# Performance work log

Measured on AMD Instinct MI355X. Metric: run time of the kernel, lower is better.

Reference implementation:

```python
import jax, jax.numpy as jnp
import numpy as np

B, T, C = 4, 2048, 1024


def wkv(k, v, w, u, reverse):
    """RWKV WKV scan with running-max stabilization.
    k, v: [B, T, C]; w, u: [C]. Returns y: [B, T, C]."""
    def step(carry, kv):
        num, den, mx = carry          # each [B, C]
        k_t, v_t = kv                 # each [B, C]
        ku = k_t + u
        m = jnp.maximum(mx, ku)
        e1 = jnp.exp(mx - m)
        e2 = jnp.exp(ku - m)
        y = (e1 * num + e2 * v_t) / (e1 * den + e2)
        # state update with decay w
        mw = mx + w
        mn = jnp.maximum(mw, k_t)
        e1s = jnp.exp(mw - mn)
        e2s = jnp.exp(k_t - mn)
        return (e1s * num + e2s * v_t, e1s * den + e2s, mn), y

    z = jnp.zeros_like(k[:, 0])
    init = (z, z, jnp.full_like(z, -1e38))
    ks = jnp.swapaxes(k, 0, 1)  # [T, B, C]
    vs = jnp.swapaxes(v, 0, 1)
    _, ys = jax.lax.scan(step, init, (ks, vs), reverse=reverse)
    return jnp.swapaxes(ys, 0, 1)


def setup_inputs() -> dict:
    key = jax.random.key(0)
    k1, k2, k3, k4, k5, k6, k7 = jax.random.split(key, 7)
    x = jax.random.normal(k1, (B, T, C), dtype=jnp.float32)
    rkv_w = jax.random.normal(k2, (6 * C, C), dtype=jnp.float32) / np.sqrt(C)
    out_w = jax.random.normal(k3, (C, 2 * C), dtype=jnp.float32) / np.sqrt(2 * C)
    time_decay = jax.random.uniform(k4, (C,), jnp.float32, -6.0, -5.0)
    time_first = jax.random.uniform(k5, (C,), jnp.float32, -3.0, 0.0)
    time_decay_rev = jax.random.uniform(k6, (C,), jnp.float32, -6.0, -5.0)
    time_first_rev = jax.random.uniform(k7, (C,), jnp.float32, -3.0, 0.0)
    return {"x": x, "rkv_w": rkv_w, "out_w": out_w,
            "time_decay": time_decay, "time_first": time_first,
            "time_decay_rev": time_decay_rev, "time_first_rev": time_first_rev}


def reference(x, rkv_w, out_w, time_decay, time_first, time_decay_rev, time_first_rev):
    b, t, c = x.shape
    rkv = jnp.einsum('btc,dc->btd', x, rkv_w).reshape(b, t, 2, 3, c)
    r_f, k_f, v_f = rkv[:, :, 0, 0], rkv[:, :, 0, 1], rkv[:, :, 0, 2]
    r_b, k_b, v_b = rkv[:, :, 1, 0], rkv[:, :, 1, 1], rkv[:, :, 1, 2]
    out_f = jax.nn.sigmoid(r_f) * wkv(k_f, v_f, -jnp.exp(time_decay), time_first, False)
    out_b = jax.nn.sigmoid(r_b) * wkv(k_b, v_b, -jnp.exp(time_decay_rev), time_first_rev, True)
    out_cat = jnp.concatenate([out_f, out_b], axis=-1)  # [B, T, 2C]
    return jnp.einsum('btd,cd->btc', out_cat, out_w)
```

## Files before the change

### kernel.cpp

```cpp
#include <hip/hip_runtime.h>
#include <cstdint>
#include <cstddef>

#define Bdim 4
#define Tdim 2048
#define Cdim 1024

#define SEG  32
#define CHB  32
#define LSEG (Tdim / SEG)

#define G1_K    1024
#define G1_GX   24
#define G1_CPX  96
#define G1_NIPT 8
#define G1_NITER 24
#define G1_GMAX 47

typedef __attribute__((ext_vector_type(8))) short bf16x8;
typedef __attribute__((ext_vector_type(4))) float f32x4;

__device__ __forceinline__ unsigned short f2bf(float f) {
    unsigned int u = __float_as_uint(f);
    u += 0x7fffu + ((u >> 16) & 1u);
    return (unsigned short)(u >> 16);
}
__device__ __forceinline__ float bf2f(unsigned short h) {
    return __uint_as_float((unsigned int)h << 16);
}

__device__ __forceinline__ void gload_lds16(const void* g, void* l) {
    __builtin_amdgcn_global_load_lds(
        (const __attribute__((address_space(1))) unsigned int*)g,
        (__attribute__((address_space(3))) unsigned int*)l,
        16, 0, 0);
}

__global__ __launch_bounds__(256) void cast_f32_bf16(
    const float* __restrict__ in, unsigned short* __restrict__ out, int n4)
{
    int i = blockIdx.x * 256 + threadIdx.x;
    if (i >= n4) return;
    float4 v = ((const float4*)in)[i];
    ushort4 o;
    o.x = f2bf(v.x); o.y = f2bf(v.y); o.z = f2bf(v.z); o.w = f2bf(v.w);
    ((ushort4*)out)[i] = o;
}

__device__ __forceinline__ void stage_half(
    const unsigned short* __restrict__ G, int row0, int K, int elemoff,
    char* slot, int wave, int lane)
{
    const int sl = (lane & 3) ^ ((lane >> 3) & 3);
    const unsigned short* gp = G + (size_t)(row0 + wave * 16 + (lane >> 2)) * K
                                 + elemoff + sl * 8;
    gload_lds16(gp, slot + wave * 1024);
    gload_lds16(gp + (size_t)128 * K, slot + 8192 + wave * 1024);
}

#define GP(D, KH, MH, GPTR, ROW0, ELEMOFF, SSLOT, VM)                          \
  {                                                                            \
    const char* As_ = ldsb + (D)*32768 + (KH)*16384;                           \
    const char* Bs_ = ldsb + 65536 + (D)*32768 + (KH)*16384;                   \
    bf16x8 a_[4], b_[4];                                                       \
    _Pragma("unroll")                                                          \
    for (int i_ = 0; i_ < 4; ++i_)                                             \
      a_[i_] = *(const bf16x8*)(As_ + (wm*128 + ((MH)*4+i_)*16 + fr)*64 + cswz);\
    _Pragma("unroll")                                                          \
    for (int j_ = 0; j_ < 4; ++j_)                                             \
      b_[j_] = *(const bf16x8*)(Bs_ + (wn*64 + j_*16 + fr)*64 + cswz);         \
    stage_half(GPTR, ROW0, G1_K, ELEMOFF, SSLOT, wave, lane);                  \
    __builtin_amdgcn_s_barrier();                                              \
    __builtin_amdgcn_sched_barrier(0);                                         \
    __builtin_amdgcn_s_setprio(1);                                             \
    _Pragma("unroll")                                                          \
    for (int i_ = 0; i_ < 4; ++i_)                                             \
      _Pragma("unroll")                                                        \
      for (int j_ = 0; j_ < 4; ++j_)                                           \
        acc[(MH)*4+i_][j_] = __builtin_amdgcn_mfma_f32_16x16x32_bf16(          \
            a_[i_], b_[j_], acc[(MH)*4+i_][j_], 0, 0, 0);                      \
    __builtin_amdgcn_s_setprio(0);                                             \
    if (VM) { asm volatile("s_waitcnt vmcnt(8)" ::: "memory"); }               \
    __builtin_amdgcn_s_barrier();                                              \
    __builtin_amdgcn_sched_barrier(0);                                         \
  }

#define SELJ(j, a0, a1, a2) ((j) == 0 ? (a0) : ((j) == 1 ? (a1) : (a2)))

__global__ __launch_bounds__(512, 1) void gemm1_persist(
    const unsigned short* __restrict__ A, const unsigned short* __restrict__ B,
    unsigned short* __restrict__ C, int N)
{
    __shared__ char ldsbuf[131072];
    char* ldsb = ldsbuf;

    const int tid  = threadIdx.x;
    const int wave = tid >> 6;
    const int lane = tid & 63;
    const int wm = wave >> 2;
    const int wn = wave & 3;
    const int fr = lane & 15;
    const int cswz = (((lane >> 4) ^ ((fr >> 1) & 3)) << 4);

    int m0j[1], n0j[1];
    int m0_0, n0_0, m0_1, n0_1, m0_2, n0_2;
    {
        int vb, swz;
        vb = blockIdx.x;          swz = (vb & 7) * G1_CPX + (vb >> 3);
        m0_0 = (swz / G1_GX) * 256; n0_0 = (swz % G1_GX) * 256;
        vb = blockIdx.x + 256;    swz = (vb & 7) * G1_CPX + (vb >> 3);
        m0_1 = (swz / G1_GX) * 256; n0_1 = (swz % G1_GX) * 256;
        vb = blockIdx.x + 512;    swz = (vb & 7) * G1_CPX + (vb >> 3);
        m0_2 = (swz / G1_GX) * 256; n0_2 = (swz % G1_GX) * 256;
    }
    (void)m0j; (void)n0j;

    f32x4 acc[8][4] = {};

    stage_half(A, m0_0, G1_K, 0,  ldsb + 0,             wave, lane);
    stage_half(B, n0_0, G1_K, 0,  ldsb + 65536,         wave, lane);
    stage_half(A, m0_0, G1_K, 32, ldsb + 16384,         wave, lane);
    stage_half(B, n0_0, G1_K, 32, ldsb + 65536 + 16384, wave, lane);
    stage_half(A, m0_0, G1_K, 64, ldsb + 32768,         wave, lane);
    stage_half(B, n0_0, G1_K, 64, ldsb + 65536 + 32768, wave, lane);
    asm volatile("s_waitcnt vmcnt(8)" ::: "memory");
    __builtin_amdgcn_s_barrier();
    __builtin_amdgcn_sched_barrier(0);

    for (int i = 0; i < G1_NITER; ++i) {
        const int jc  = i >> 3;
        int g2 = 2 * i + 2; if (g2 > G1_GMAX) g2 = G1_GMAX;
        int g3 = 2 * i + 3; if (g3 > G1_GMAX) g3 = G1_GMAX;
        const int j2 = g2 >> 4, kt2 = g2 & 15;
        const int j3 = g3 >> 4, kt3 = g3 & 15;
        const int kt1 = (2 * i + 1) & 15;

        const int m0c = SELJ(jc, m0_0, m0_1, m0_2);
        const int n0c = SELJ(jc, n0_0, n0_1, n0_2);
        const int m02 = SELJ(j2, m0_0, m0_1, m0_2);
        const int n02 = SELJ(j2, n0_0, n0_1, n0_2);
        const int m03 = SELJ(j3, m0_0, m0_1, m0_2);
        const int n03 = SELJ(j3, n0_0, n0_1, n0_2);

        GP(0, 0, 0, A, m0c, kt1 * 64 + 32, ldsb + 32768 + 16384,         0)
        GP(0, 0, 1, B, n0c, kt1 * 64 + 32, ldsb + 65536 + 32768 + 16384, 1)
        GP(0, 1, 0, A, m02, kt2 * 64,      ldsb + 0,                     0)
        GP(0, 1, 1, B, n02, kt2 * 64,      ldsb + 65536,                 1)
        GP(1, 0, 0, A, m02, kt2 * 64 + 32, ldsb + 16384,                 0)
        GP(1, 0, 1, B, n02, kt2 * 64 + 32, ldsb + 65536 + 16384,         1)
        GP(1, 1, 0, A, m03, kt3 * 64,      ldsb + 32768,                 0)
        GP(1, 1, 1, B, n03, kt3 * 64,      ldsb + 65536 + 32768,         1)

        if ((i & 7) == 7) {
            #pragma unroll
            for (int mi = 0; mi < 8; ++mi) {
                const int row = m0c + wm * 128 + mi * 16 + (lane >> 4) * 4;
                #pragma unroll
                for (int nj = 0; nj < 4; ++nj) {
                    const int col = n0c + wn * 64 + nj * 16 + fr;
                    #pragma unroll
                    for (int r = 0; r < 4; ++r)
                        C[(size_t)(row + r) * N + col] = f2bf(acc[mi][nj][r]);
                }
            }
            #pragma unroll
            for (int mi = 0; mi < 8; ++mi)
                #pragma unroll
                for (int nj = 0; nj < 4; ++nj)
                    acc[mi][nj] = (f32x4){0.f, 0.f, 0.f, 0.f};
        }
    }
}

__global__ __launch_bounds__(256) void gemm_bf16_nt(
    const unsigned short* __restrict__ A, const unsigned short* __restrict__ B,
    float* __restrict__ C, int M, int N, int K)
{
    __shared__ unsigned short As[128 * 32];
    __shared__ unsigned short Bs[128 * 32];

    const int tid  = threadIdx.x;
    const int wave = tid >> 6;
    const int lane = tid & 63;
    const int m0 = blockIdx.y * 128;
    const int n0 = blockIdx.x * 128;
    const int wr = wave >> 1, wc = wave & 1;

    const int srow = tid >> 2;
    const int scol = (tid & 3) * 8;
    const unsigned short* Ag = A + (size_t)(m0 + srow) * K + scol;
    const unsigned short* Bg = B + (size_t)(n0 + srow) * K + scol;
    char* AsW = (char*)As + wave * 1024;
    char* BsW = (char*)Bs + wave * 1024;

    f32x4 acc[4][4] = {};

    const int fr = lane & 15;
    const int fk = (lane >> 4) * 8;

    for (int k0 = 0; k0 < K; k0 += 32) {
        gload_lds16(Ag + k0,                  AsW);
        gload_lds16(Ag + k0 + (size_t)64 * K, AsW + 4096);
        gload_lds16(Bg + k0,                  BsW);
        gload_lds16(Bg + k0 + (size_t)64 * K, BsW + 4096);
        __syncthreads();

        bf16x8 af[4], bfr_[4];
        #pragma unroll
        for (int f = 0; f < 4; ++f) {
            af[f]   = *(const bf16x8*)&As[(wr * 64 + f * 16 + fr) * 32 + fk];
            bfr_[f] = *(const bf16x8*)&Bs[(wc * 64 + f * 16 + fr) * 32 + fk];
        }
        #pragma unroll
        for (int i = 0; i < 4; ++i)
            #pragma unroll
            for (int j = 0; j < 4; ++j)
                acc[i][j] = __builtin_amdgcn_mfma_f32_16x16x32_bf16(
                    af[i], bfr_[j], acc[i][j], 0, 0, 0);
        __syncthreads();
    }

    #pragma unroll
    for (int i = 0; i < 4; ++i) {
        const int row = m0 + wr * 64 + i * 16 + (lane >> 4) * 4;
        #pragma unroll
        for (int j = 0; j < 4; ++j) {
            const int col = n0 + wc * 64 + j * 16 + (lane & 15);
            #pragma unroll
            for (int r = 0; r < 4; ++r)
                C[(size_t)(row + r) * N + col] = acc[i][j][r];
        }
    }
}

__global__ __launch_bounds__(1024) void wkv_scan_par(
    const unsigned short* __restrict__ rkv,
    const float* __restrict__ td,  const float* __restrict__ tf,
    const float* __restrict__ tdr, const float* __restrict__ tfr,
    unsigned short* __restrict__ outcat)
{
    __shared__ float sBn[SEG][CHB], sBd[SEG][CHB], sMb[SEG][CHB];

    const int tid = threadIdx.x;
    const int ch  = tid & (CHB - 1);
    const int seg = tid >> 5;

    const int bi  = blockIdx.x;
    const int b   = bi >> 6;
    const int rem = bi & 63;
    const int dir = rem >> 5;
    const int c   = (rem & 31) * CHB + ch;

    const float w = -__expf(dir ? tdr[c] : td[c]);
    const float u = dir ? tfr[c] : tf[c];

    const int strideT = 6 * Cdim;
    const int tstep   = dir ? -strideT : strideT;
    const int t0      = dir ? (Tdim - 1 - seg * LSEG) : (seg * LSEG);

    const unsigned short* pbase = rkv + ((size_t)b * Tdim + t0) * strideT + dir * 3 * Cdim + c;

    const int PF = 8;

    float bn = 0.0f, bd = 0.0f, mb = -1e38f;
    {
        const unsigned short* q = pbase;
        float kk[PF], vv[PF];
        #pragma unroll
        for (int i = 0; i < PF; ++i) {
            kk[i] = bf2f(q[Cdim]); vv[i] = bf2f(q[2 * Cdim]); q += tstep;
        }
        for (int t = 0; t < LSEG; t += PF) {
            float kn[PF], vn[PF];
            if (t + PF < LSEG) {
                #pragma unroll
                for (int i = 0; i < PF; ++i) {
                    kn[i] = bf2f(q[Cdim]); vn[i] = bf2f(q[2 * Cdim]); q += tstep;
                }
            }
            #pragma unroll
            for (int i = 0; i < PF; ++i) {
                const float k_ = kk[i], v_ = vv[i];
                const float mw = mb + w;
                const float mn = fmaxf(mw, k_);
                const float e1 = __expf(mw - mn);
                const float e2 = __expf(k_ - mn);
                bn = e1 * bn + e2 * v_;
                bd = e1 * bd + e2;
                mb = mn;
            }
            #pragma unroll
            for (int i = 0; i < PF; ++i) { kk[i] = kn[i]; vv[i] = vn[i]; }
        }
    }
    sBn[seg][ch] = bn; sBd[seg][ch] = bd; sMb[seg][ch] = mb;
    __syncthreads();

    if (tid < CHB) {
        float n = 0.0f, d = 0.0f, m = -1e38f;
        const float a = w * (float)LSEG;
        for (int s = 0; s < SEG; ++s) {
            const float tn = sBn[s][tid], tdn = sBd[s][tid], tm = sMb[s][tid];
            sBn[s][tid] = n; sBd[s][tid] = d; sMb[s][tid] = m;
            const float ma = m + a;
            const float mm = fmaxf(ma, tm);
            const float e1 = __expf(ma - mm);
            const float e2 = __expf(tm - mm);
            n = e1 * n + e2 * tn;
            d = e1 * d + e2 * tdn;
            m = mm;
        }
    }
    __syncthreads();

    float num = sBn[seg][ch], den = sBd[seg][ch], mx = sMb[seg][ch];
    {
        const unsigned short* q = pbase;
        unsigned short* po = outcat + ((size_t)b * Tdim + t0) * (2 * Cdim) + dir * Cdim + c;
        const int ostep = dir ? -(2 * Cdim) : (2 * Cdim);

        float rr[PF], kk[PF], vv[PF];
        #pragma unroll
        for (int i = 0; i < PF; ++i) {
            rr[i] = bf2f(q[0]); kk[i] = bf2f(q[Cdim]); vv[i] = bf2f(q[2 * Cdim]); q += tstep;
        }
        for (int t = 0; t < LSEG; t += PF) {
            float rn[PF], kn[PF], vn[PF];
            if (t + PF < LSEG) {
                #pragma unroll
                for (int i = 0; i < PF; ++i) {
                    rn[i] = bf2f(q[0]); kn[i] = bf2f(q[Cdim]); vn[i] = bf2f(q[2 * Cdim]); q += tstep;
                }
            }
            #pragma unroll
            for (int i = 0; i < PF; ++i) {
                const float k_ = kk[i], v_ = vv[i], r_ = rr[i];
                const float ku = k_ + u;
                const float m  = fmaxf(mx, ku);
                const float e1 = __expf(mx - m);
                const float e2 = __expf(ku - m);
                const float y  = (e1 * num + e2 * v_) / (e1 * den + e2);
                const float sr = 1.0f / (1.0f + __expf(-r_));
                *po = f2bf(sr * y);
                po += ostep;
                const float mw  = mx + w;
                const float mn  = fmaxf(mw, k_);
                const float e1s = __expf(mw - mn);
                const float e2s = __expf(k_ - mn);
                num = e1s * num + e2s * v_;
                den = e1s * den + e2s;
                mx  = mn;
            }
            #pragma unroll
            for (int i = 0; i < PF; ++i) { rr[i] = rn[i]; kk[i] = kn[i]; vv[i] = vn[i]; }
        }
    }
}

extern "C" void kernel_launch(void* const* d_in, const int* in_sizes, int n_in,
                              void* d_out, int out_size, void* d_ws, size_t ws_size,
                              hipStream_t stream)
{
    const float* x    = (const float*)d_in[0];
    const float* rkvw = (const float*)d_in[1];
    const float* outw = (const float*)d_in[2];
    const float* td   = (const float*)d_in[3];
    const float* tf   = (const float*)d_in[4];
    const float* tdr  = (const float*)d_in[5];
    const float* tfr  = (const float*)d_in[6];
    float* out = (float*)d_out;

    const int M = Bdim * Tdim;

    char* ws = (char*)d_ws;
    unsigned short* rkv = (unsigned short*)ws;
    unsigned short* xb  = (unsigned short*)(ws + 100663296);
    unsigned short* wb  = (unsigned short*)(ws + 117440512);
    unsigned short* ob  = (unsigned short*)(ws + 130023424);
    unsigned short* cat = (unsigned short*)(ws + 134217728);

    dim3 blk(256);

    hipLaunchKernelGGL(cast_f32_bf16, dim3((M * Cdim / 4 + 255) / 256), blk, 0, stream,
                       x, xb, M * Cdim / 4);
    hipLaunchKernelGGL(cast_f32_bf16, dim3((6 * Cdim * Cdim / 4 + 255) / 256), blk, 0, stream,
                       rkvw, wb, 6 * Cdim * Cdim / 4);
    hipLaunchKernelGGL(cast_f32_bf16, dim3((Cdim * 2 * Cdim / 4 + 255) / 256), blk, 0, stream,
                       outw, ob, Cdim * 2 * Cdim / 4);

    hipLaunchKernelGGL(gemm1_persist, dim3(256), dim3(512), 0, stream,
                       xb, wb, rkv, 6 * Cdim);

    hipLaunchKernelGGL(wkv_scan_par, dim3(Bdim * 2 * (Cdim / CHB)), dim3(1024), 0, stream,
                       rkv, td, tf, tdr, tfr, cat);

    hipLaunchKernelGGL(gemm_bf16_nt, dim3(Cdim / 128, M / 128), blk, 0, stream,
                       cat, ob, out, M, Cdim, 2 * Cdim);
}
```

Measured before the change: 253.5 us.

## Software-pipeline LDS fragment reads ahead of MFMA phases in persistent GEMM

Restructures the GEMM main loop so A fragments for the next MFMA phase are read from LDS before the current phase's barrier, using double register buffers (aX/aY). B fragments are now loaded once per K-half and reused across both M-halves. The global-load wait threshold also drops from vmcnt(8) to vmcnt(6). This aims to hide LDS read latency behind MFMA work at the cost of extra VGPRs. The earlier prefetch and the final read of the next buffer need to be correctly ordered against the LDS staging writes.

```diff
diff --git a/kernel.cpp b/kernel.cpp
--- a/kernel.cpp
+++ b/kernel.cpp
@@ -13,7 +13,6 @@
 #define G1_K    1024
 #define G1_GX   24
 #define G1_CPX  96
-#define G1_NIPT 8
 #define G1_NITER 24
 #define G1_GMAX 47
 
@@ -58,32 +57,32 @@
     gload_lds16(gp + (size_t)128 * K, slot + 8192 + wave * 1024);
 }
 
-#define GP(D, KH, MH, GPTR, ROW0, ELEMOFF, SSLOT, VM)                          \
+#define RD_A(DST, D, KH, MHOFF)                                                \
   {                                                                            \
     const char* As_ = ldsb + (D)*32768 + (KH)*16384;                           \
-    const char* Bs_ = ldsb + 65536 + (D)*32768 + (KH)*16384;                   \
-    bf16x8 a_[4], b_[4];                                                       \
     _Pragma("unroll")                                                          \
     for (int i_ = 0; i_ < 4; ++i_)                                             \
-      a_[i_] = *(const bf16x8*)(As_ + (wm*128 + ((MH)*4+i_)*16 + fr)*64 + cswz);\
+      DST[i_] = *(const bf16x8*)(As_ + (wm*128 + (MHOFF) + i_*16 + fr)*64 + cswz); \
+  }
+#define RD_B(D, KH)                                                            \
+  {                                                                            \
+    const char* Bs_ = ldsb + 65536 + (D)*32768 + (KH)*16384;                   \
     _Pragma("unroll")                                                          \
     for (int j_ = 0; j_ < 4; ++j_)                                             \
-      b_[j_] = *(const bf16x8*)(Bs_ + (wn*64 + j_*16 + fr)*64 + cswz);         \
-    stage_half(GPTR, ROW0, G1_K, ELEMOFF, SSLOT, wave, lane);                  \
-    __builtin_amdgcn_s_barrier();                                              \
-    __builtin_amdgcn_sched_barrier(0);                                         \
+      bq[j_] = *(const bf16x8*)(Bs_ + (wn*64 + j_*16 + fr)*64 + cswz);         \
+  }
+#define MM(SRC, ACCOFF)                                                        \
     __builtin_amdgcn_s_setprio(1);                                             \
     _Pragma("unroll")                                                          \
     for (int i_ = 0; i_ < 4; ++i_)                                             \
       _Pragma("unroll")                                                        \
       for (int j_ = 0; j_ < 4; ++j_)                                           \
-        acc[(MH)*4+i_][j_] = __builtin_amdgcn_mfma_f32_16x16x32_bf16(          \
-            a_[i_], b_[j_], acc[(MH)*4+i_][j_], 0, 0, 0);                      \
-    __builtin_amdgcn_s_setprio(0);                                             \
-    if (VM) { asm volatile("s_waitcnt vmcnt(8)" ::: "memory"); }               \
-    __builtin_amdgcn_s_barrier();                                              \
-    __builtin_amdgcn_sched_barrier(0);                                         \
-  }
+        acc[(ACCOFF)+i_][j_] = __builtin_amdgcn_mfma_f32_16x16x32_bf16(        \
+            SRC[i_], bq[j_], acc[(ACCOFF)+i_][j_], 0, 0, 0);                   \
+    __builtin_amdgcn_s_setprio(0);
+
+#define BARS  __builtin_amdgcn_s_barrier(); __builtin_amdgcn_sched_barrier(0);
+#define VM6   asm volatile("s_waitcnt vmcnt(6)" ::: "memory");
 
 #define SELJ(j, a0, a1, a2) ((j) == 0 ? (a0) : ((j) == 1 ? (a1) : (a2)))
 
@@ -102,7 +101,6 @@
     const int fr = lane & 15;
     const int cswz = (((lane >> 4) ^ ((fr >> 1) & 3)) << 4);
 
-    int m0j[1], n0j[1];
     int m0_0, n0_0, m0_1, n0_1, m0_2, n0_2;
     {
         int vb, swz;
@@ -113,9 +111,9 @@
         vb = blockIdx.x + 512;    swz = (vb & 7) * G1_CPX + (vb >> 3);
         m0_2 = (swz / G1_GX) * 256; n0_2 = (swz % G1_GX) * 256;
     }
-    (void)m0j; (void)n0j;
 
     f32x4 acc[8][4] = {};
+    bf16x8 aX[4], aY[4], bq[4];
 
     stage_half(A, m0_0, G1_K, 0,  ldsb + 0,             wave, lane);
     stage_half(B, n0_0, G1_K, 0,  ldsb + 65536,         wave, lane);
@@ -126,6 +124,7 @@
     asm volatile("s_waitcnt vmcnt(8)" ::: "memory");
     __builtin_amdgcn_s_barrier();
     __builtin_amdgcn_sched_barrier(0);
+    RD_A(aX, 0, 0, 0)
 
     for (int i = 0; i < G1_NITER; ++i) {
         const int jc  = i >> 3;
@@ -142,14 +141,30 @@
         const int m03 = SELJ(j3, m0_0, m0_1, m0_2);
         const int n03 = SELJ(j3, n0_0, n0_1, n0_2);
 
-        GP(0, 0, 0, A, m0c, kt1 * 64 + 32, ldsb + 32768 + 16384,         0)
-        GP(0, 0, 1, B, n0c, kt1 * 64 + 32, ldsb + 65536 + 32768 + 16384, 1)
-        GP(0, 1, 0, A, m02, kt2 * 64,      ldsb + 0,                     0)
-        GP(0, 1, 1, B, n02, kt2 * 64,      ldsb + 65536,                 1)
-        GP(1, 0, 0, A, m02, kt2 * 64 + 32, ldsb + 16384,                 0)
-        GP(1, 0, 1, B, n02, kt2 * 64 + 32, ldsb + 65536 + 16384,         1)
-        GP(1, 1, 0, A, m03, kt3 * 64,      ldsb + 32768,                 0)
-        GP(1, 1, 1, B, n03, kt3 * 64,      ldsb + 65536 + 32768,         1)
+        RD_B(0, 0) RD_A(aY, 0, 0, 64)
+        stage_half(A, m0c, G1_K, kt1 * 64 + 32, ldsb + 32768 + 16384, wave, lane);
+        BARS  MM(aX, 0)  BARS
+        RD_A(aX, 0, 1, 0)
+        stage_half(B, n0c, G1_K, kt1 * 64 + 32, ldsb + 65536 + 32768 + 16384, wave, lane);
+        BARS  MM(aY, 4)  VM6  BARS
+        RD_B(0, 1) RD_A(aY, 0, 1, 64)
+        stage_half(A, m02, G1_K, kt2 * 64, ldsb + 0, wave, lane);
+        BARS  MM(aX, 0)  BARS
+        RD_A(aX, 1, 0, 0)
+        stage_half(B, n02, G1_K, kt2 * 64, ldsb + 65536, wave, lane);
+        BARS  MM(aY, 4)  VM6  BARS
+        RD_B(1, 0) RD_A(aY, 1, 0, 64)
+        stage_half(A, m02, G1_K, kt2 * 64 + 32, ldsb + 16384, wave, lane);
+        BARS  MM(aX, 0)  BARS
+        RD_A(aX, 1, 1, 0)
+        stage_half(B, n02, G1_K, kt2 * 64 + 32, ldsb + 65536 + 16384, wave, lane);
+        BARS  MM(aY, 4)  VM6  BARS
+        RD_B(1, 1) RD_A(aY, 1, 1, 64)
+        stage_half(A, m03, G1_K, kt3 * 64, ldsb + 32768, wave, lane);
+        BARS  MM(aX, 0)  BARS
+        RD_A(aX, 0, 0, 0)
+        stage_half(B, n03, G1_K, kt3 * 64, ldsb + 65536 + 32768, wave, lane);
+        BARS  MM(aY, 4)  VM6  BARS
 
         if ((i & 7) == 7) {
             #pragma unroll
```

Result: no change. 252.0 us (-0.6%).
